# Kernel tuning notes

Hardware: AMD Instinct MI355X
Metric: run time of the kernel (lower is better)

Reference implementation:

```python
import jax, jax.numpy as jnp
import numpy as np

B, S, E, A = 4, 2048, 1024, 64  # batch, seq, embedding_size, attention_size


def setup_inputs() -> dict:
    key = jax.random.key(0)
    k1, k2 = jax.random.split(key)
    embedding = jax.random.normal(k1, (B, S, E), dtype=jnp.float32)
    # nn.Linear(embedding_size, attention_size, bias=False).weight has shape [A, E]
    Wk = jax.random.normal(k2, (A, E), dtype=jnp.float32) * (1.0 / np.sqrt(E))
    return {"embedding": embedding, "Wk": Wk}


def reference(embedding, Wk):
    # NOTE: the original module (buggily) calls self.key() for q, k, AND v.
    # We reproduce that math faithfully: q = k = v = embedding @ Wk.T.
    k = jnp.einsum('bse,ae->bsa', embedding, Wk)  # [B,S,A]
    q = k
    v = k
    x = jnp.einsum('bqa,bka->bqk', q, k) / jnp.sqrt(jnp.float32(A))  # [B,S,S]
    # Faithful to masked_fill(torch.tril(x) == 0, -inf): masks the strict upper
    # triangle (tril zeros it) plus any lower-triangle entries exactly equal to 0.
    x = jnp.where(jnp.tril(x) == 0, -jnp.inf, x)
    x = jax.nn.softmax(x, axis=2)
    return jnp.einsum('bqk,bka->bqa', x, v)  # [B,S,A]
```

## Files before the change

kernel.cpp:

```cpp
#include <hip/hip_runtime.h>
#include <math.h>

#define BATCH 4
#define SLEN  2048
#define EMB   1024
#define AH    64

typedef __attribute__((ext_vector_type(8))) short bf16x8;
typedef __attribute__((ext_vector_type(4))) float f32x4;

#define MFMA16(a, b, c) __builtin_amdgcn_mfma_f32_16x16x32_bf16((a), (b), (c), 0, 0, 0)

__device__ __forceinline__ void async16(const void* g, void* l) {
  __builtin_amdgcn_global_load_lds(
      (const __attribute__((address_space(1))) unsigned int*)g,
      (__attribute__((address_space(3))) unsigned int*)l, 16, 0, 0);
}

__device__ __forceinline__ short f2bf(float x) {
  union { float f; unsigned u; } v; v.f = x;
  unsigned r = v.u + 0x7fffu + ((v.u >> 16) & 1u);
  return (short)(r >> 16);
}
__device__ __forceinline__ float bf2f(short h) {
  union { unsigned u; float f; } v; v.u = ((unsigned)(unsigned short)h) << 16;
  return v.f;
}

__device__ __forceinline__ void split_trunc(float4 a0, float4 a1, bf16x8& hi, bf16x8& lo) {
  unsigned c[8] = {__float_as_uint(a0.x), __float_as_uint(a0.y), __float_as_uint(a0.z),
                   __float_as_uint(a0.w), __float_as_uint(a1.x), __float_as_uint(a1.y),
                   __float_as_uint(a1.z), __float_as_uint(a1.w)};
  union { bf16x8 v; unsigned d[4]; } H, L;
  H.d[0] = __builtin_amdgcn_perm(c[1], c[0], 0x07060302u);
  H.d[1] = __builtin_amdgcn_perm(c[3], c[2], 0x07060302u);
  H.d[2] = __builtin_amdgcn_perm(c[5], c[4], 0x07060302u);
  H.d[3] = __builtin_amdgcn_perm(c[7], c[6], 0x07060302u);
  unsigned e[8];
#pragma unroll
  for (int j = 0; j < 8; ++j)
    e[j] = __float_as_uint(__uint_as_float(c[j]) - __uint_as_float(c[j] & 0xffff0000u));
  L.d[0] = __builtin_amdgcn_perm(e[1], e[0], 0x07060302u);
  L.d[1] = __builtin_amdgcn_perm(e[3], e[2], 0x07060302u);
  L.d[2] = __builtin_amdgcn_perm(e[5], e[4], 0x07060302u);
  L.d[3] = __builtin_amdgcn_perm(e[7], e[6], 0x07060302u);
  hi = H.v; lo = L.v;
}

__device__ __forceinline__ int slot_off(int qt) {
  return (qt == 0) ? 0 : qt + (((qt - 1) * (qt - 1)) >> 2);
}

#define CH_SHORTS 24576

__global__ __launch_bounds__(256) void prep_wk_kernel(const float* __restrict__ Wk,
                                                      short* __restrict__ BpkG) {
  int tg = blockIdx.x * 256 + threadIdx.x;
  int kc = tg >> 8, rem = tg & 255, nt = rem >> 6, lane = rem & 63;
  int n = nt * 16 + (lane & 15);
  int k = kc * 32 + (lane >> 4) * 8;
  const float* src = Wk + (size_t)n * EMB + k;
  float4 a0 = *(const float4*)src;
  float4 a1 = *(const float4*)(src + 4);
  bf16x8 hi, lo;
  split_trunc(a0, a1, hi, lo);
  short* dst = BpkG + ((size_t)(kc * 4 + nt) * 128 + lane) * 8;
  *(bf16x8*)dst = hi;
  *(bf16x8*)(dst + 512) = lo;
}

__global__ __launch_bounds__(256) void gemm_k_kernel(const float* __restrict__ emb,
                                                     const short* __restrict__ BpkG,
                                                     short* __restrict__ Kpack) {
  __shared__ __align__(16) char glds[40960];

  const int t = threadIdx.x;
  const int w = t >> 6, l = t & 63, lm = l & 15, quad = l >> 4;
  const int nt = w;
  const int row0 = blockIdx.x * 16;

  auto stage = [&](int step, int bs) {
    char* base = glds + bs * 20480;
    float* eT = (float*)base;
    short* bT = (short*)(base + 4096);
    int rowl = 4 * w + (l >> 4);
    int du = (l & 15) ^ (rowl & 7);
    async16(emb + (size_t)(row0 + rowl) * EMB + step * 64 + du * 4, eT + w * 256);
    const short* bg = BpkG + (size_t)step * 8192;
#pragma unroll
    for (int u = 0; u < 4; ++u)
      async16(bg + (w * 4 + u) * 512 + l * 8, bT + (w * 4 + u) * 512);
  };

  f32x4 acc = {0.f, 0.f, 0.f, 0.f};
  stage(0, 0);
#pragma unroll
  for (int s = 0; s < 16; ++s) {
    __syncthreads();
    if (s < 15) stage(s + 1, (s + 1) & 1);
    char* base = glds + (s & 1) * 20480;
    float* eT = (float*)base;
    short* bT = (short*)(base + 4096);
#pragma unroll
    for (int kc = 0; kc < 2; ++kc) {
      int du0 = kc * 8 + quad * 2;
      float4 a0 = *(const float4*)((char*)eT + lm * 256 + ((du0) ^ (lm & 7)) * 16);
      float4 a1 = *(const float4*)((char*)eT + lm * 256 + ((du0 + 1) ^ (lm & 7)) * 16);
      bf16x8 ahi, alo;
      split_trunc(a0, a1, ahi, alo);
      bf16x8 bhi = *(const bf16x8*)(bT + (((kc * 4 + nt) * 2 + 0) * 64 + l) * 8);
      bf16x8 blo = *(const bf16x8*)(bT + (((kc * 4 + nt) * 2 + 1) * 64 + l) * 8);
      acc = MFMA16(ahi, bhi, acc);
      acc = MFMA16(ahi, blo, acc);
      acc = MFMA16(alo, bhi, acc);
    }
  }

  const int a = nt * 16 + lm;
#pragma unroll
  for (int r = 0; r < 4; ++r) {
    int srow = row0 + quad * 4 + r;
    float v = acc[r];
    short h = f2bf(v);
    short lo2 = f2bf(v - bf2f(h));
    int bb = srow >> 11, si = srow & 2047, c = si >> 7, key = si & 127;
    int kb = key >> 4, klm = key & 15;
    size_t cb = (size_t)(bb * 16 + c) * CH_SHORTS;
    size_t kbo = (size_t)((kb * 2 + (a >> 5)) * 64 + ((a & 31) >> 3) * 16 + klm) * 8 + (a & 7);
    Kpack[cb + kbo] = h;
    Kpack[cb + 8192 + kbo] = lo2;
    size_t vbo = (size_t)(((key >> 5) * 4 + (a >> 4)) * 64 + ((key & 31) >> 3) * 16 + (a & 15)) * 8 + (key & 7);
    Kpack[cb + 16384 + vbo] = h;
  }
}

__global__ __launch_bounds__(256, 3) void flash_kernel(const short* __restrict__ Kpack,
                                                       short* __restrict__ OpartH,
                                                       float2* __restrict__ mlpart) {
  const int c = blockIdx.x, qt = blockIdx.y, b = blockIdx.z;
  if (2 * c > qt) return;

  __shared__ __align__(16) short KLs[16384];
  __shared__ __align__(16) short Plds[4][16][132];

  const int t = threadIdx.x;
  const int w = t >> 6, l = t & 63, lm = l & 15, quad = l >> 4;
  const int k0 = c * 128;
  const int qr0 = qt * 64 + w * 16;

  const short* chunkG = Kpack + (size_t)(b * 16 + c) * CH_SHORTS;
#pragma unroll
  for (int u = 0; u < 8; ++u) {
    int slot = w * 8 + u;
    async16(chunkG + slot * 512 + l * 8, KLs + slot * 512);
  }

  const short* qG = Kpack + (size_t)(b * 16 + (qt >> 1)) * CH_SHORTS + ((qt & 1) * 4 + w) * 1024;
  bf16x8 qh0 = *(const bf16x8*)(qG + l * 8);
  bf16x8 qh1 = *(const bf16x8*)(qG + 512 + l * 8);
  bf16x8 ql0 = *(const bf16x8*)(qG + 8192 + l * 8);
  bf16x8 ql1 = *(const bf16x8*)(qG + 8192 + 512 + l * 8);

  bf16x8 vf[4][4];
#pragma unroll
  for (int kc2 = 0; kc2 < 4; ++kc2)
#pragma unroll
    for (int nt = 0; nt < 4; ++nt)
      vf[kc2][nt] = *(const bf16x8*)(chunkG + 16384 + ((kc2 * 4 + nt) * 64 + l) * 8);

  __syncthreads();

  f32x4 sc[8];
#pragma unroll
  for (int kg = 0; kg < 8; ++kg) {
    bf16x8 bh0 = *(const bf16x8*)(KLs + ((kg * 2 + 0) * 64 + l) * 8);
    bf16x8 bh1 = *(const bf16x8*)(KLs + ((kg * 2 + 1) * 64 + l) * 8);
    bf16x8 bl0 = *(const bf16x8*)(KLs + 8192 + ((kg * 2 + 0) * 64 + l) * 8);
    bf16x8 bl1 = *(const bf16x8*)(KLs + 8192 + ((kg * 2 + 1) * 64 + l) * 8);
    f32x4 s = {0.f, 0.f, 0.f, 0.f};
    s = MFMA16(qh0, bh0, s);
    s = MFMA16(qh0, bl0, s);
    s = MFMA16(ql0, bh0, s);
    s = MFMA16(qh1, bh1, s);
    s = MFMA16(qh1, bl1, s);
    s = MFMA16(ql1, bh1, s);
    sc[kg] = s;
  }

  float rm[4] = {-INFINITY, -INFINITY, -INFINITY, -INFINITY};
#pragma unroll
  for (int kg = 0; kg < 8; ++kg) {
    const int col = k0 + kg * 16 + lm;
#pragma unroll
    for (int r = 0; r < 4; ++r) {
      const int row = qr0 + quad * 4 + r;
      float v = sc[kg][r] * 0.125f;
      v = (col > row || v == 0.0f) ? -INFINITY : v;
      sc[kg][r] = v;
      rm[r] = fmaxf(rm[r], v);
    }
  }
  float m_i[4], l_i[4];
#pragma unroll
  for (int r = 0; r < 4; ++r) {
    for (int off = 1; off < 16; off <<= 1) rm[r] = fmaxf(rm[r], __shfl_xor(rm[r], off, 16));
    m_i[r] = rm[r];
  }
  float rs[4] = {0.f, 0.f, 0.f, 0.f};
#pragma unroll
  for (int kg = 0; kg < 8; ++kg)
#pragma unroll
    for (int r = 0; r < 4; ++r) {
      float p = (sc[kg][r] == -INFINITY) ? 0.f : __expf(sc[kg][r] - m_i[r]);
      sc[kg][r] = p;
      rs[r] += p;
    }
#pragma unroll
  for (int r = 0; r < 4; ++r) {
    for (int off = 1; off < 16; off <<= 1) rs[r] += __shfl_xor(rs[r], off, 16);
    l_i[r] = rs[r];
  }

#pragma unroll
  for (int kg = 0; kg < 8; ++kg)
#pragma unroll
    for (int r = 0; r < 4; ++r)
      Plds[w][quad * 4 + r][kg * 16 + lm] = f2bf(sc[kg][r]);

  f32x4 o[4] = {{0.f,0.f,0.f,0.f},{0.f,0.f,0.f,0.f},{0.f,0.f,0.f,0.f},{0.f,0.f,0.f,0.f}};
#pragma unroll
  for (int kc2 = 0; kc2 < 4; ++kc2) {
    bf16x8 pf = *(const bf16x8*)&Plds[w][lm][kc2 * 32 + quad * 8];
#pragma unroll
    for (int nt = 0; nt < 4; ++nt)
      o[nt] = MFMA16(pf, vf[kc2][nt], o[nt]);
  }

  const int slot = b * 272 + slot_off(qt) + c;
  short* Ob = OpartH + (size_t)slot * 4096;
#pragma unroll
  for (int nt = 0; nt < 4; ++nt)
#pragma unroll
    for (int r = 0; r < 4; ++r)
      Ob[(size_t)(w * 16 + quad * 4 + r) * AH + nt * 16 + lm] = f2bf(o[nt][r]);
  if (lm == 0) {
#pragma unroll
    for (int r = 0; r < 4; ++r)
      mlpart[(size_t)slot * 64 + w * 16 + quad * 4 + r] = make_float2(m_i[r], l_i[r]);
  }
}

__global__ __launch_bounds__(256) void merge_kernel(const short* __restrict__ OpartH,
                                                    const float2* __restrict__ mlpart,
                                                    float* __restrict__ out) {
  __shared__ __align__(16) short ldsO[16 * 1024];
  __shared__ float wtab[16][17];
  const int t = threadIdx.x;
  const int w = t >> 6, l = t & 63;
  const int rg = blockIdx.x, qt = blockIdx.y, b = blockIdx.z;
  const int r0 = rg * 16;
  const int nch = (qt >> 1) + 1;
  const int slotbase = b * 272 + slot_off(qt);

#pragma unroll
  for (int u = 0; u < 8; ++u) {
    int idx = w * 8 + u;
    int c = idx >> 1, half = idx & 1;
    if (c < nch)
      async16(OpartH + (size_t)(slotbase + c) * 4096 + r0 * 64 + half * 512 + l * 8,
              ldsO + c * 1024 + half * 512 + l * 8);
  }

  const int row = w * 4 + (l >> 4), c = l & 15;
  float mc = -INFINITY, lc = 0.f;
  if (c < nch) {
    float2 ml = mlpart[(size_t)(slotbase + c) * 64 + r0 + row];
    mc = ml.x; lc = ml.y;
  }
  float M = mc;
  for (int off = 1; off < 16; off <<= 1) M = fmaxf(M, __shfl_xor(M, off, 16));
  float wgt = (mc != -INFINITY) ? __expf(mc - M) : 0.f;
  float L = lc * wgt;
  for (int off = 1; off < 16; off <<= 1) L += __shfl_xor(L, off, 16);
  wtab[row][c] = wgt / L;

  __syncthreads();

  const int row2 = t >> 4, a0 = (t & 15) * 4;
  float4 acc = make_float4(0.f, 0.f, 0.f, 0.f);
  for (int cc = 0; cc < nch; ++cc) {
    float wv = wtab[row2][cc];
    short4 v4 = *(const short4*)(ldsO + cc * 1024 + row2 * 64 + a0);
    acc.x += wv * bf2f(v4.x); acc.y += wv * bf2f(v4.y);
    acc.z += wv * bf2f(v4.z); acc.w += wv * bf2f(v4.w);
  }
  *(float4*)&out[((size_t)(b * 2048 + qt * 64 + r0 + row2)) * AH + a0] = acc;
}

extern "C" void kernel_launch(void* const* d_in, const int* in_sizes, int n_in,
                              void* d_out, int out_size, void* d_ws, size_t ws_size,
                              hipStream_t stream) {
  const float* emb = (const float*)d_in[0];
  const float* Wk  = (const float*)d_in[1];
  float* out = (float*)d_out;
  char* ws = (char*)d_ws;

  short*  Kpack  = (short*)(ws);
  short*  BpkG   = (short*)(ws + 3145728);
  short*  OpartH = (short*)(ws + 3670016);
  float2* mlpart = (float2*)(ws + 12582912);

  prep_wk_kernel<<<dim3(32), dim3(256), 0, stream>>>(Wk, BpkG);
  gemm_k_kernel<<<dim3(512), dim3(256), 0, stream>>>(emb, BpkG, Kpack);
  flash_kernel<<<dim3(16, 32, 4), dim3(256), 0, stream>>>(Kpack, OpartH, mlpart);
  merge_kernel<<<dim3(4, 32, 4), dim3(256), 0, stream>>>(OpartH, mlpart, out);
}
```

Measured before the change: 105.4 us.

## Fuse four kernels into one persistent ticketed megakernel with dataflow flags

Merges the prep, GEMM, flash-attention and merge kernels into a single launch. Blocks claim work in dependency order through an atomic ticket counter and spin on per-chunk and per-query-tile flags, so later stages can start as soon as their own inputs are ready. The intent is to remove the launch gaps and tail drain between stages and to drop the flash kernel's early-exit empty blocks. In exchange it adds a flag-reset launch, spin-wait latency, a shared-memory union sized for the largest stage, and a bounded spin that could silently proceed on stale data if a wait times out.

New measurement: 333.3 us. 3.16x slower.

```diff
diff --git a/kernel.cpp b/kernel.cpp
--- a/kernel.cpp
+++ b/kernel.cpp
@@ -53,9 +53,17 @@
 
 #define CH_SHORTS 24576
 
-__global__ __launch_bounds__(256) void prep_wk_kernel(const float* __restrict__ Wk,
-                                                      short* __restrict__ BpkG) {
-  int tg = blockIdx.x * 256 + threadIdx.x;
+
+union __align__(16) SMem {
+  char glds[40960];
+  struct { short KLs[16384]; short Plds[4][16][132]; } f;
+  struct { short ldsO[16384]; float wtab[16][17]; } m;
+};
+
+
+__device__ __forceinline__ void prep_body(int item, const float* __restrict__ Wk,
+                                          short* __restrict__ BpkG) {
+  int tg = item * 256 + (int)threadIdx.x;
   int kc = tg >> 8, rem = tg & 255, nt = rem >> 6, lane = rem & 63;
   int n = nt * 16 + (lane & 15);
   int k = kc * 32 + (lane >> 4) * 8;
@@ -69,15 +77,14 @@
   *(bf16x8*)(dst + 512) = lo;
 }
 
-__global__ __launch_bounds__(256) void gemm_k_kernel(const float* __restrict__ emb,
-                                                     const short* __restrict__ BpkG,
-                                                     short* __restrict__ Kpack) {
-  __shared__ __align__(16) char glds[40960];
-
+__device__ __forceinline__ void gemm_body(int blk, const float* __restrict__ emb,
+                                          const short* __restrict__ BpkG,
+                                          short* __restrict__ Kpack, SMem& sm) {
+  char* glds = sm.glds;
   const int t = threadIdx.x;
   const int w = t >> 6, l = t & 63, lm = l & 15, quad = l >> 4;
   const int nt = w;
-  const int row0 = blockIdx.x * 16;
+  const int row0 = blk * 16;
 
   auto stage = [&](int step, int bs) {
     char* base = glds + bs * 20480;
@@ -134,14 +141,12 @@
   }
 }
 
-__global__ __launch_bounds__(256, 3) void flash_kernel(const short* __restrict__ Kpack,
-                                                       short* __restrict__ OpartH,
-                                                       float2* __restrict__ mlpart) {
-  const int c = blockIdx.x, qt = blockIdx.y, b = blockIdx.z;
-  if (2 * c > qt) return;
-
-  __shared__ __align__(16) short KLs[16384];
-  __shared__ __align__(16) short Plds[4][16][132];
+__device__ __forceinline__ void flash_body(int c, int qt, int b,
+                                           const short* __restrict__ Kpack,
+                                           short* __restrict__ OpartH,
+                                           float2* __restrict__ mlpart, SMem& sm) {
+  auto& KLs = sm.f.KLs;
+  auto& Plds = sm.f.Plds;
 
   const int t = threadIdx.x;
   const int w = t >> 6, l = t & 63, lm = l & 15, quad = l >> 4;
@@ -250,14 +255,14 @@
   }
 }
 
-__global__ __launch_bounds__(256) void merge_kernel(const short* __restrict__ OpartH,
-                                                    const float2* __restrict__ mlpart,
-                                                    float* __restrict__ out) {
-  __shared__ __align__(16) short ldsO[16 * 1024];
-  __shared__ float wtab[16][17];
+__device__ __forceinline__ void merge_body(int rg, int qt, int b,
+                                           const short* __restrict__ OpartH,
+                                           const float2* __restrict__ mlpart,
+                                           float* __restrict__ out, SMem& sm) {
+  auto& ldsO = sm.m.ldsO;
+  auto& wtab = sm.m.wtab;
   const int t = threadIdx.x;
   const int w = t >> 6, l = t & 63;
-  const int rg = blockIdx.x, qt = blockIdx.y, b = blockIdx.z;
   const int r0 = rg * 16;
   const int nch = (qt >> 1) + 1;
   const int slotbase = b * 272 + slot_off(qt);
@@ -297,6 +302,76 @@
   *(float4*)&out[((size_t)(b * 2048 + qt * 64 + r0 + row2)) * AH + a0] = acc;
 }
 
+
+__device__ __forceinline__ void signal(int* p) {
+  __syncthreads();
+  if (threadIdx.x == 0) {
+    __threadfence();
+    __hip_atomic_fetch_add(p, 1, __ATOMIC_RELEASE, __HIP_MEMORY_SCOPE_AGENT);
+  }
+}
+
+__device__ __forceinline__ void spin_ge(int* p, int target) {
+  for (int i = 0; i < (1 << 20); ++i) {
+    if (__hip_atomic_load(p, __ATOMIC_ACQUIRE, __HIP_MEMORY_SCOPE_AGENT) >= target) return;
+    __builtin_amdgcn_s_sleep(2);
+  }
+}
+
+__device__ __forceinline__ void wait_ge(int* p, int target) {
+  if (threadIdx.x == 0) spin_ge(p, target);
+  __syncthreads();
+}
+
+__global__ void reset_flags(int* __restrict__ flags) {
+  flags[threadIdx.x] = 0;
+}
+
+__global__ __launch_bounds__(256, 3) void mega_kernel(
+    const float* __restrict__ emb, const float* __restrict__ Wk,
+    short* __restrict__ BpkG, short* __restrict__ Kpack,
+    short* __restrict__ OpartH, float2* __restrict__ mlpart,
+    float* __restrict__ out, int* __restrict__ flags) {
+  __shared__ SMem sm;
+  __shared__ int s_tk;
+  const int t = threadIdx.x;
+  if (t == 0)
+    s_tk = __hip_atomic_fetch_add(&flags[0], 1, __ATOMIC_RELAXED, __HIP_MEMORY_SCOPE_AGENT);
+  __syncthreads();
+  const int tk = s_tk;
+
+  if (tk < 32) {
+    prep_body(tk, Wk, BpkG);
+    signal(&flags[1]);
+  } else if (tk < 544) {
+    const int g = tk - 32;
+    wait_ge(&flags[1], 32);
+    gemm_body(g, emb, BpkG, Kpack, sm);
+    signal(&flags[2 + (g >> 3)]);
+  } else if (tk < 1632) {
+    const int fitem = tk - 544;
+    const int b = fitem / 272;
+    const int r = fitem % 272;
+    int qt = (int)(2.0f * sqrtf((float)r + 1.0f));
+    if (qt > 31) qt = 31;
+    while (slot_off(qt) > r) --qt;
+    while (qt < 31 && slot_off(qt + 1) <= r) ++qt;
+    const int c = r - slot_off(qt);
+    if (t == 0) {
+      spin_ge(&flags[2 + b * 16 + c], 8);
+      spin_ge(&flags[2 + b * 16 + (qt >> 1)], 8);
+    }
+    __syncthreads();
+    flash_body(c, qt, b, Kpack, OpartH, mlpart, sm);
+    signal(&flags[66 + b * 32 + qt]);
+  } else {
+    const int m = tk - 1632;
+    const int b = m >> 7, qt = (m >> 2) & 31, rg = m & 3;
+    wait_ge(&flags[66 + b * 32 + qt], (qt >> 1) + 1);
+    merge_body(rg, qt, b, OpartH, mlpart, out, sm);
+  }
+}
+
 extern "C" void kernel_launch(void* const* d_in, const int* in_sizes, int n_in,
                               void* d_out, int out_size, void* d_ws, size_t ws_size,
                               hipStream_t stream) {
@@ -309,9 +384,9 @@
   short*  BpkG   = (short*)(ws + 3145728);
   short*  OpartH = (short*)(ws + 3670016);
   float2* mlpart = (float2*)(ws + 12582912);
-
-  prep_wk_kernel<<<dim3(32), dim3(256), 0, stream>>>(Wk, BpkG);
-  gemm_k_kernel<<<dim3(512), dim3(256), 0, stream>>>(emb, BpkG, Kpack);
-  flash_kernel<<<dim3(16, 32, 4), dim3(256), 0, stream>>>(Kpack, OpartH, mlpart);
-  merge_kernel<<<dim3(4, 32, 4), dim3(256), 0, stream>>>(OpartH, mlpart, out);
-}
+  int*    flags  = (int*)(ws + 13139968);
+
+  reset_flags<<<dim3(1), dim3(256), 0, stream>>>(flags);
+  mega_kernel<<<dim3(2144), dim3(256), 0, stream>>>(emb, Wk, BpkG, Kpack, OpartH,
+                                                    mlpart, out, flags);
+}
```

## Preload whole embedding tile to LDS and read K-low/B fragments from global

Applied to the files above, without the earlier changes.

The K-projection GEMM now loads all 16 k-steps of the embedding tile into 64KB LDS in one go with a single barrier, and reads packed Wk fragments directly from global memory instead of double-buffering both through LDS. The flash kernel halves its K tile in LDS by reading the low-part K fragments straight from global, and raises the occupancy hint from 3 to 4 blocks per SM. The aim is to cut barriers and LDS footprint so more blocks stay resident. The cost is losing load/compute overlap in the GEMM and adding latency from more global loads.

Result: slower. 112.4 us (+6.6%).

```diff
diff --git a/kernel.cpp b/kernel.cpp
--- a/kernel.cpp
+++ b/kernel.cpp
@@ -52,6 +52,7 @@
 }
 
 #define CH_SHORTS 24576
+
 
 __global__ __launch_bounds__(256) void prep_wk_kernel(const float* __restrict__ Wk,
                                                       short* __restrict__ BpkG) {
@@ -72,44 +73,37 @@
 __global__ __launch_bounds__(256) void gemm_k_kernel(const float* __restrict__ emb,
                                                      const short* __restrict__ BpkG,
                                                      short* __restrict__ Kpack) {
-  __shared__ __align__(16) char glds[40960];
+  __shared__ __align__(16) float eT[16384];
 
   const int t = threadIdx.x;
   const int w = t >> 6, l = t & 63, lm = l & 15, quad = l >> 4;
   const int nt = w;
   const int row0 = blockIdx.x * 16;
 
-  auto stage = [&](int step, int bs) {
-    char* base = glds + bs * 20480;
-    float* eT = (float*)base;
-    short* bT = (short*)(base + 4096);
+  {
     int rowl = 4 * w + (l >> 4);
     int du = (l & 15) ^ (rowl & 7);
-    async16(emb + (size_t)(row0 + rowl) * EMB + step * 64 + du * 4, eT + w * 256);
-    const short* bg = BpkG + (size_t)step * 8192;
-#pragma unroll
-    for (int u = 0; u < 4; ++u)
-      async16(bg + (w * 4 + u) * 512 + l * 8, bT + (w * 4 + u) * 512);
-  };
+    const float* src = emb + (size_t)(row0 + rowl) * EMB + du * 4;
+#pragma unroll
+    for (int s = 0; s < 16; ++s)
+      async16(src + s * 64, eT + s * 1024 + w * 256);
+  }
+  __syncthreads();
 
   f32x4 acc = {0.f, 0.f, 0.f, 0.f};
-  stage(0, 0);
 #pragma unroll
   for (int s = 0; s < 16; ++s) {
-    __syncthreads();
-    if (s < 15) stage(s + 1, (s + 1) & 1);
-    char* base = glds + (s & 1) * 20480;
-    float* eT = (float*)base;
-    short* bT = (short*)(base + 4096);
+    const char* eS = (const char*)(eT + s * 1024);
+    const short* bg = BpkG + (size_t)s * 8192;
 #pragma unroll
     for (int kc = 0; kc < 2; ++kc) {
       int du0 = kc * 8 + quad * 2;
-      float4 a0 = *(const float4*)((char*)eT + lm * 256 + ((du0) ^ (lm & 7)) * 16);
-      float4 a1 = *(const float4*)((char*)eT + lm * 256 + ((du0 + 1) ^ (lm & 7)) * 16);
+      float4 a0 = *(const float4*)(eS + lm * 256 + ((du0) ^ (lm & 7)) * 16);
+      float4 a1 = *(const float4*)(eS + lm * 256 + ((du0 + 1) ^ (lm & 7)) * 16);
       bf16x8 ahi, alo;
       split_trunc(a0, a1, ahi, alo);
-      bf16x8 bhi = *(const bf16x8*)(bT + (((kc * 4 + nt) * 2 + 0) * 64 + l) * 8);
-      bf16x8 blo = *(const bf16x8*)(bT + (((kc * 4 + nt) * 2 + 1) * 64 + l) * 8);
+      bf16x8 bhi = *(const bf16x8*)(bg + (((kc * 4 + nt) * 2 + 0) * 64 + l) * 8);
+      bf16x8 blo = *(const bf16x8*)(bg + (((kc * 4 + nt) * 2 + 1) * 64 + l) * 8);
       acc = MFMA16(ahi, bhi, acc);
       acc = MFMA16(ahi, blo, acc);
       acc = MFMA16(alo, bhi, acc);
@@ -134,13 +128,13 @@
   }
 }
 
-__global__ __launch_bounds__(256, 3) void flash_kernel(const short* __restrict__ Kpack,
+__global__ __launch_bounds__(256, 4) void flash_kernel(const short* __restrict__ Kpack,
                                                        short* __restrict__ OpartH,
                                                        float2* __restrict__ mlpart) {
   const int c = blockIdx.x, qt = blockIdx.y, b = blockIdx.z;
   if (2 * c > qt) return;
 
-  __shared__ __align__(16) short KLs[16384];
+  __shared__ __align__(16) short KLs[8192];
   __shared__ __align__(16) short Plds[4][16][132];
 
   const int t = threadIdx.x;
@@ -150,8 +144,8 @@
 
   const short* chunkG = Kpack + (size_t)(b * 16 + c) * CH_SHORTS;
 #pragma unroll
-  for (int u = 0; u < 8; ++u) {
-    int slot = w * 8 + u;
+  for (int u = 0; u < 4; ++u) {
+    int slot = w * 4 + u;
     async16(chunkG + slot * 512 + l * 8, KLs + slot * 512);
   }
 
@@ -175,8 +169,8 @@
   for (int kg = 0; kg < 8; ++kg) {
     bf16x8 bh0 = *(const bf16x8*)(KLs + ((kg * 2 + 0) * 64 + l) * 8);
     bf16x8 bh1 = *(const bf16x8*)(KLs + ((kg * 2 + 1) * 64 + l) * 8);
-    bf16x8 bl0 = *(const bf16x8*)(KLs + 8192 + ((kg * 2 + 0) * 64 + l) * 8);
-    bf16x8 bl1 = *(const bf16x8*)(KLs + 8192 + ((kg * 2 + 1) * 64 + l) * 8);
+    bf16x8 bl0 = *(const bf16x8*)(chunkG + 8192 + ((kg * 2 + 0) * 64 + l) * 8);
+    bf16x8 bl1 = *(const bf16x8*)(chunkG + 8192 + ((kg * 2 + 1) * 64 + l) * 8);
     f32x4 s = {0.f, 0.f, 0.f, 0.f};
     s = MFMA16(qh0, bh0, s);
     s = MFMA16(qh0, bl0, s);
```
